# Kernel tuning notes

Hardware: AMD Instinct MI355X
Metric: run time of the kernel (lower is better)

Reference implementation:

```python
import jax, jax.numpy as jnp
import numpy as np

ALPHA = 0.2  # LeakyReLU negative slope
NEG_INF = -1.0e12


def setup_inputs() -> dict:
    key = jax.random.key(0)
    ks = jax.random.split(key, 8)
    N, F, D, H, M, Q = 4096, 512, 64, 4, 2, 128
    x = jax.random.normal(ks[0], (N, F), dtype=jnp.float32)
    adj = jax.random.randint(ks[1], (M, N, N), 0, 2, dtype=jnp.int32)
    W = jax.random.normal(ks[2], (H, F, D), dtype=jnp.float32) * 0.07
    a1 = jax.random.normal(ks[3], (H, D), dtype=jnp.float32) * 0.15
    a2 = jax.random.normal(ks[4], (H, D), dtype=jnp.float32) * 0.15
    Ws = jax.random.normal(ks[5], (H * D, Q), dtype=jnp.float32) * 0.1
    bs = jax.random.normal(ks[6], (1, Q), dtype=jnp.float32) * 0.1
    q_sem = jax.random.normal(ks[7], (Q, 1), dtype=jnp.float32) * 0.15
    return {"x": x, "adj": adj, "W": W, "a1": a1, "a2": a2,
            "Ws": Ws, "bs": bs, "q_sem": q_sem}


def reference(x, adj, W, a1, a2, Ws, bs, q_sem):
    N = x.shape[0]
    # Wh is identical across meta-paths (dropout disabled / eval mode)
    Wh = jnp.einsum('nf,hfd->hnd', x, W)            # [H,N,D]
    s1 = jnp.einsum('hnd,hd->hn', Wh, a1)           # Wh @ a[:D]
    s2 = jnp.einsum('hnd,hd->hn', Wh, a2)           # Wh @ a[D:]

    def metapath(adj_m):
        # e[h,i,j] = leaky_relu(s1[h,i] + s2[h,j]); mask by adjacency
        e = jax.nn.leaky_relu(s1[:, :, None] + s2[:, None, :], negative_slope=ALPHA)
        e = jnp.where(adj_m[None, :, :] > 0, e, NEG_INF)
        att = jax.nn.softmax(e, axis=2)             # softmax over neighbors (dim=1 in torch [N,N])
        h = jax.nn.elu(jnp.einsum('hnm,hmd->hnd', att, Wh))
        return jnp.transpose(h, (1, 0, 2)).reshape(N, -1)  # concat heads -> [N, H*D]

    Z = jax.vmap(metapath)(adj)                     # [M, N, H*D]
    z = jnp.transpose(Z, (1, 0, 2))                 # [N, M, H*D]

    # Semantic attention (faithful to original, incl. softmax over dim=1 of [M,1])
    Whs = jnp.tanh(jnp.einsum('nmf,fq->nmq', z, Ws) + bs)   # [N,M,Q]
    w = jnp.einsum('nmq,qo->nmo', Whs, q_sem).mean(0)        # [M,1]
    beta = jax.nn.softmax(w, axis=1)                          # [M,1]
    return (beta[None, :, :] * z).sum(axis=1)                 # [N, H*D]
```

## Files before the change

kernel.cpp:

```cpp
#include <hip/hip_runtime.h>
#include <hip/hip_fp16.h>
#include <stdint.h>

#define NN 4096
#define FF 512
#define DD 64
#define HH 4
#define MM 2
#define LOG2E 1.44269504088896340736f
#define ALPHA_LR 0.2f

typedef float f32x4 __attribute__((ext_vector_type(4)));
typedef _Float16 f16x8 __attribute__((ext_vector_type(8)));
typedef _Float16 f16x2 __attribute__((ext_vector_type(2)));
typedef unsigned short u16x2 __attribute__((ext_vector_type(2)));

extern "C" __device__ _Float16 __ocml_exp2_f16(_Float16);

union H4 { ushort4 u; _Float16 h[4]; };
union W8 { f16x8 v; uint32_t w[4]; f16x2 p[4]; };

__device__ inline float fast_exp2(float x) { return __builtin_amdgcn_exp2f(x); }
__device__ inline float fast_rcp(float x) { return __builtin_amdgcn_rcpf(x); }
__device__ inline f32x4 mfma16(f16x8 a, f16x8 b, f32x4 c) {
    return __builtin_amdgcn_mfma_f32_16x16x32_f16(a, b, c, 0, 0, 0);
}
__device__ inline uint32_t enc_f32(float f) {
    uint32_t u = __float_as_uint(f);
    return (u & 0x80000000u) ? ~u : (u | 0x80000000u);
}
__device__ inline float dec_f32(uint32_t k) {
    uint32_t u = (k & 0x80000000u) ? (k ^ 0x80000000u) : ~k;
    return __uint_as_float(u);
}
__device__ inline f16x2 msk01(uint32_t V, int k) {
    uint32_t w = (V >> (2 * k)) & 0x00010001u;
    u16x2 m = __builtin_bit_cast(u16x2, w) * (u16x2){0x3C00, 0x3C00};
    return __builtin_bit_cast(f16x2, m);
}
__device__ inline f16x2 pkmax(f16x2 a, f16x2 b) {
#if __has_builtin(__builtin_elementwise_max)
    return __builtin_elementwise_max(a, b);
#else
    return (f16x2){a[0] > b[0] ? a[0] : b[0], a[1] > b[1] ? a[1] : b[1]};
#endif
}

#define GLOAD_LDS(G, L)                                                     \
    __builtin_amdgcn_global_load_lds(                                       \
        (const __attribute__((address_space(1))) void*)(G),                 \
        (__attribute__((address_space(3))) void*)(L), 16, 0, 0)

__global__ __launch_bounds__(256) void k_prep(const int* __restrict__ adj,
                                              const float* __restrict__ W,
                                              _Float16* __restrict__ wt,
                                              unsigned long long* __restrict__ bitsT,
                                              uint32_t* __restrict__ m4a) {
    const int bid = blockIdx.x;
    if (bid < 2048) {
        const long long total = (long long)MM * NN * NN;
        const long long stride = 2048LL * 256;
        long long tid = (long long)bid * 256 + threadIdx.x;
        for (long long e = tid; e < total; e += stride) {
            unsigned long long msk = __ballot(adj[e] != 0);
            if ((threadIdx.x & 63) == 0) {
                long long q = e >> 6;
                int m  = (int)(q >> 18);
                int rem = (int)(q & 262143);
                int i  = rem >> 6;
                int jw = rem & 63;
                bitsT[((size_t)m * 64 + jw) * NN + i] = msk;
            }
        }
    } else {
        int t = (bid - 2048) * 256 + threadIdx.x;
        if (t < HH) m4a[t] = 0u;
        int c = t >> 9, f = t & 511;
        int h = c >> 6, d = c & 63;
        wt[t] = (_Float16)W[(h * FF + f) * DD + d];
    }
}

__global__ __launch_bounds__(512) void k_wh(const float* __restrict__ x,
                                            const _Float16* __restrict__ wt,
                                            const float* __restrict__ a1,
                                            const float* __restrict__ a2,
                                            _Float16* __restrict__ whT,
                                            float* __restrict__ s1L,
                                            _Float16* __restrict__ s2h,
                                            uint32_t* __restrict__ m4a) {
    __shared__ float sred[8][2][16];
    const int wave = threadIdx.x >> 6;
    const int h    = wave & 3;
    const int th   = wave >> 2;
    const int lane = threadIdx.x & 63;
    const int iL   = lane & 15;
    const int quad = lane >> 4;
    const int i0   = blockIdx.x * 16;

    f32x4 acc[2];
    acc[0] = (f32x4){0.f, 0.f, 0.f, 0.f};
    acc[1] = (f32x4){0.f, 0.f, 0.f, 0.f};

    const float* arow = x + (size_t)(i0 + iL) * FF + quad * 8;
    const _Float16* bbase = wt + (size_t)(h * 64 + th * 32 + iL) * FF + quad * 8;

    for (int kc = 0; kc < FF; kc += 32) {
        f32x4 xa = *(const f32x4*)(arow + kc);
        f32x4 xb = *(const f32x4*)(arow + kc + 4);
        f16x8 a;
        #pragma unroll
        for (int r = 0; r < 4; ++r) {
            a[r]     = (_Float16)xa[r];
            a[4 + r] = (_Float16)xb[r];
        }
        #pragma unroll
        for (int u = 0; u < 2; ++u) {
            f16x8 b = *(const f16x8*)(bbase + (size_t)(16 * u) * FF + kc);
            acc[u] = mfma16(a, b, acc[u]);
        }
    }
    #pragma unroll
    for (int u = 0; u < 2; ++u) {
        H4 o;
        #pragma unroll
        for (int r = 0; r < 4; ++r) o.h[r] = (_Float16)acc[u][r];
        *(ushort4*)(whT + (size_t)(h * 64 + th * 32 + 16 * u + iL) * NN + i0 + quad * 4) = o.u;
    }

    const float a1v0 = a1[h * 64 + th * 32 + iL];
    const float a1v1 = a1[h * 64 + th * 32 + 16 + iL];
    const float a2v0 = a2[h * 64 + th * 32 + iL];
    const float a2v1 = a2[h * 64 + th * 32 + 16 + iL];
    #pragma unroll
    for (int r = 0; r < 4; ++r) {
        float p1 = acc[0][r] * a1v0 + acc[1][r] * a1v1;
        float p2 = acc[0][r] * a2v0 + acc[1][r] * a2v1;
        #pragma unroll
        for (int off = 1; off < 16; off <<= 1) {
            p1 += __shfl_xor(p1, off);
            p2 += __shfl_xor(p2, off);
        }
        if (iL == 0) {
            sred[wave][0][quad * 4 + r] = p1;
            sred[wave][1][quad * 4 + r] = p2;
        }
    }
    __syncthreads();
    if (threadIdx.x < 64) {
        int h2  = threadIdx.x >> 4;
        int idx = threadIdx.x & 15;
        float s1 = sred[h2][0][idx] + sred[h2 + 4][0][idx];
        float s2 = sred[h2][1][idx] + sred[h2 + 4][1][idx];
        float s2l = s2 * LOG2E;
        s1L[h2 * NN + i0 + idx] = s1 * LOG2E;
        s2h[h2 * NN + i0 + idx] = (_Float16)s2l;
        float mx = s2l;
        #pragma unroll
        for (int off = 1; off < 16; off <<= 1) mx = fmaxf(mx, __shfl_xor(mx, off));
        if (idx == 0) atomicMax(m4a + h2, enc_f32(mx));
    }
}

__global__ __launch_bounds__(512, 1) void k_attn(const _Float16* __restrict__ whT,
                                                 const float* __restrict__ s1L,
                                                 const _Float16* __restrict__ s2h,
                                                 const uint32_t* __restrict__ m4a,
                                                 const unsigned long long* __restrict__ bitsT,
                                                 float* __restrict__ out) {
    union __align__(16) Smem {
        _Float16 stage[8][2][4096];
        struct {
            float xr[8][MM][4][16][16];
            float dr[8][MM][16];
        } epi;
    };
    __shared__ Smem sm;

    const int tid  = threadIdx.x;
    const int wave = tid >> 6;
    const int lane = tid & 63;
    const int iL   = lane & 15;
    const int quad = lane >> 4;
    const int h    = blockIdx.x & 3;
    const int i0   = (blockIdx.x >> 2) * 64;

    const float m4 = dec_f32(m4a[h]);
    f16x2 A2[4], B2[4];
    #pragma unroll
    for (int s = 0; s < 4; ++s) {
        float s1i = s1L[h * NN + i0 + 16 * s + iL];
        float vv  = s1i + m4;
        float cii = fmaxf(vv, ALPHA_LR * vv);
        _Float16 a = (_Float16)(s1i - cii);
        _Float16 b = (_Float16)(ALPHA_LR * s1i - cii);
        A2[s] = (f16x2){a, a};
        B2[s] = (f16x2){b, b};
    }
    const f16x2 al2 = (f16x2){(_Float16)ALPHA_LR, (_Float16)ALPHA_LR};

    f32x4 acc[4][MM][4];
    f32x4 accD[4][MM];
    #pragma unroll
    for (int s = 0; s < 4; ++s)
        #pragma unroll
        for (int m = 0; m < MM; ++m) {
            accD[s][m] = (f32x4){0.f, 0.f, 0.f, 0.f};
            #pragma unroll
            for (int t = 0; t < 4; ++t) acc[s][m][t] = (f32x4){0.f, 0.f, 0.f, 0.f};
        }

    f16x8 bones;
    #pragma unroll
    for (int e = 0; e < 8; ++e) bones[e] = (_Float16)1.0f;

    const _Float16* s2row = s2h + h * NN;
    const int qshift = quad * 8;
    const int jbase = wave * 512;

    const _Float16* stBase = whT
        + (size_t)(h * 64 + (lane >> 3)) * NN
        + (((lane & 7) ^ ((lane >> 3) & 7)) << 3);
    const int x3 = iL & 7;
    int rdOff[2];
    #pragma unroll
    for (int hf = 0; hf < 2; ++hf)
        rdOff[hf] = (iL << 7) + ((((hf << 2) + quad) ^ x3) << 4);

    _Float16* cur = &sm.stage[wave][0][0];
    _Float16* nxt = &sm.stage[wave][1][0];

    const unsigned long long* pB[MM][4];
    #pragma unroll
    for (int m = 0; m < MM; ++m)
        #pragma unroll
        for (int s = 0; s < 4; ++s)
            pB[m][s] = bitsT + (size_t)m * 64 * NN + i0 + 16 * s + iL;

    {
        const _Float16* src = stBase + jbase;
        #pragma unroll
        for (int k = 0; k < 8; ++k)
            GLOAD_LDS(src + (size_t)(k * 8) * NN, cur + k * 512);
    }
    asm volatile("s_waitcnt vmcnt(0)" ::: "memory");
    __builtin_amdgcn_sched_barrier(0);

    #pragma unroll 1
    for (int it = 0; it < 8; ++it) {
        const int jc = jbase + it * 64;
        const int jw = jc >> 6;
        unsigned long long bm[MM][4];
        #pragma unroll
        for (int m = 0; m < MM; ++m)
            #pragma unroll
            for (int s = 0; s < 4; ++s)
                bm[m][s] = pB[m][s][(size_t)jw * NN];
        W8 s2vh[2];
        s2vh[0].v = *(const f16x8*)(s2row + jc + qshift);
        s2vh[1].v = *(const f16x8*)(s2row + jc + 32 + qshift);

        __builtin_amdgcn_sched_barrier(0);
        if (it < 7) {
            const _Float16* src = stBase + (jc + 64);
            #pragma unroll
            for (int k = 0; k < 8; ++k)
                GLOAD_LDS(src + (size_t)(k * 8) * NN, nxt + k * 512);
        }
        __builtin_amdgcn_sched_barrier(0);

        #pragma unroll
        for (int half = 0; half < 2; ++half) {
            const int shft = 32 * half + qshift;
            f16x8 bfr[4];
            #pragma unroll
            for (int t = 0; t < 4; ++t)
                bfr[t] = *(const f16x8*)((const char*)cur + (t << 11) + rdOff[half]);

            #pragma unroll
            for (int s = 0; s < 4; ++s) {
                uint32_t rs0 = (uint32_t)(bm[0][s] >> shft) & 0xFFu;
                uint32_t rs1 = (uint32_t)(bm[1][s] >> shft) & 0xFFu;
                uint32_t V0 = rs0 | (rs0 << 15);
                uint32_t V1 = rs1 | (rs1 << 15);
                W8 a0, a1v;
                #pragma unroll
                for (int k = 0; k < 4; ++k) {
                    f16x2 z = s2vh[half].p[k] + A2[s];
                    f16x2 l = al2 * s2vh[half].p[k] + B2[s];
                    f16x2 mx = pkmax(z, l);
                    f16x2 p = (f16x2){__ocml_exp2_f16(mx[0]), __ocml_exp2_f16(mx[1])};
                    a0.p[k]  = p * msk01(V0, k);
                    a1v.p[k] = p * msk01(V1, k);
                }
                #pragma unroll
                for (int t = 0; t < 4; ++t) {
                    acc[s][0][t] = mfma16(a0.v, bfr[t], acc[s][0][t]);
                    acc[s][1][t] = mfma16(a1v.v, bfr[t], acc[s][1][t]);
                }
                accD[s][0] = mfma16(a0.v, bones, accD[s][0]);
                accD[s][1] = mfma16(a1v.v, bones, accD[s][1]);
            }
        }

        asm volatile("s_waitcnt vmcnt(0)" ::: "memory");
        __builtin_amdgcn_sched_barrier(0);
        _Float16* tmp = cur; cur = nxt; nxt = tmp;
    }

    #pragma unroll
    for (int s = 0; s < 4; ++s) {
        __syncthreads();
        #pragma unroll
        for (int m = 0; m < MM; ++m) {
            #pragma unroll
            for (int t = 0; t < 4; ++t)
                *(f32x4*)&sm.epi.xr[wave][m][t][iL][quad * 4] = acc[s][m][t];
            if (iL == 0) *(f32x4*)&sm.epi.dr[wave][m][quad * 4] = accD[s][m];
        }
        __syncthreads();
        if (wave < 4) {
            const int t = wave;
            f32x4 n0 = (f32x4){0.f, 0.f, 0.f, 0.f};
            f32x4 n1 = (f32x4){0.f, 0.f, 0.f, 0.f};
            f32x4 d0 = (f32x4){0.f, 0.f, 0.f, 0.f};
            f32x4 d1 = (f32x4){0.f, 0.f, 0.f, 0.f};
            #pragma unroll
            for (int sl = 0; sl < 8; ++sl) {
                n0 += *(const f32x4*)&sm.epi.xr[sl][0][t][iL][quad * 4];
                n1 += *(const f32x4*)&sm.epi.xr[sl][1][t][iL][quad * 4];
                d0 += *(const f32x4*)&sm.epi.dr[sl][0][quad * 4];
                d1 += *(const f32x4*)&sm.epi.dr[sl][1][quad * 4];
            }
            const int i0s = i0 + 16 * s;
            #pragma unroll
            for (int r = 0; r < 4; ++r) {
                float v0 = n0[r] * fast_rcp(d0[r]);
                float v1 = n1[r] * fast_rcp(d1[r]);
                float e0 = v0 > 0.f ? v0 : (fast_exp2(v0 * LOG2E) - 1.f);
                float e1 = v1 > 0.f ? v1 : (fast_exp2(v1 * LOG2E) - 1.f);
                out[(size_t)(i0s + quad * 4 + r) * (HH * DD) + h * 64 + 16 * t + iL] = e0 + e1;
            }
        }
    }
}

extern "C" void kernel_launch(void* const* d_in, const int* in_sizes, int n_in,
                              void* d_out, int out_size, void* d_ws, size_t ws_size,
                              hipStream_t stream) {
    const float* x   = (const float*)d_in[0];
    const int*   adj = (const int*)d_in[1];
    const float* W   = (const float*)d_in[2];
    const float* a1  = (const float*)d_in[3];
    const float* a2  = (const float*)d_in[4];
    float* out = (float*)d_out;

    char* ws = (char*)d_ws;
    _Float16* wt   = (_Float16*)(ws);
    _Float16* whT  = (_Float16*)(ws + 262144);
    float*    s1L  = (float*)(ws + 2359296);
    _Float16* s2h  = (_Float16*)(ws + 2424832);
    uint32_t* m4a  = (uint32_t*)(ws + 2457600);
    unsigned long long* bitsT = (unsigned long long*)(ws + 2490368);

    hipLaunchKernelGGL(k_prep, dim3(2560), dim3(256), 0, stream,
                       adj, W, wt, bitsT, m4a);
    hipLaunchKernelGGL(k_wh, dim3(256), dim3(512), 0, stream,
                       x, wt, a1, a2, whT, s1L, s2h, m4a);
    hipLaunchKernelGGL(k_attn, dim3(256), dim3(512), 0, stream,
                       whT, s1L, s2h, m4a, bitsT, out);
}
```

Measured before the change: 270.9 us.

## Factor attention exponent into precomputed per-row and per-column exp terms

Rewrites exp2(max(s1+s2 terms)) as max(U1[i]*e1[j], U2[i]*ea[j]), using the monotonicity of exp. The per-column factors exp2(s2-m) and exp2(alpha*(s2-m)) are computed once per wave into LDS, and the per-row factors once per thread. This removes two f16 transcendentals per score element from the inner loop, leaving packed multiplies and a max. The cost is extra LDS reads each half-iteration and a risk of fp16 underflow or precision loss in the products.

```diff
diff --git a/kernel.cpp b/kernel.cpp
--- a/kernel.cpp
+++ b/kernel.cpp
@@ -14,8 +14,6 @@
 typedef _Float16 f16x8 __attribute__((ext_vector_type(8)));
 typedef _Float16 f16x2 __attribute__((ext_vector_type(2)));
 typedef unsigned short u16x2 __attribute__((ext_vector_type(2)));
-
-extern "C" __device__ _Float16 __ocml_exp2_f16(_Float16);
 
 union H4 { ushort4 u; _Float16 h[4]; };
 union W8 { f16x8 v; uint32_t w[4]; f16x2 p[4]; };
@@ -168,12 +166,16 @@
                                                  const uint32_t* __restrict__ m4a,
                                                  const unsigned long long* __restrict__ bitsT,
                                                  float* __restrict__ out) {
-    union __align__(16) Smem {
-        _Float16 stage[8][2][4096];
-        struct {
-            float xr[8][MM][4][16][16];
-            float dr[8][MM][16];
-        } epi;
+    struct __align__(16) Smem {
+        union {
+            _Float16 stage[8][2][4096];
+            struct {
+                float xr[8][MM][4][16][16];
+                float dr[8][MM][16];
+            } epi;
+        };
+        _Float16 e1[8][512];
+        _Float16 ea[8][512];
     };
     __shared__ Smem sm;
 
@@ -185,19 +187,35 @@
     const int h    = blockIdx.x & 3;
     const int i0   = (blockIdx.x >> 2) * 64;
 
+    const int qshift = quad * 8;
+    const int jbase = wave * 512;
+
     const float m4 = dec_f32(m4a[h]);
-    f16x2 A2[4], B2[4];
+
+    {
+        f16x8 sv = *(const f16x8*)(s2h + h * NN + jbase + lane * 8);
+        f16x8 e1v8, eav8;
+        #pragma unroll
+        for (int e = 0; e < 8; ++e) {
+            float sf = (float)sv[e] - m4;
+            e1v8[e] = (_Float16)fast_exp2(sf);
+            eav8[e] = (_Float16)fast_exp2(ALPHA_LR * sf);
+        }
+        *(f16x8*)&sm.e1[wave][lane * 8] = e1v8;
+        *(f16x8*)&sm.ea[wave][lane * 8] = eav8;
+    }
+
+    f16x2 U1[4], U2[4];
     #pragma unroll
     for (int s = 0; s < 4; ++s) {
         float s1i = s1L[h * NN + i0 + 16 * s + iL];
         float vv  = s1i + m4;
         float cii = fmaxf(vv, ALPHA_LR * vv);
-        _Float16 a = (_Float16)(s1i - cii);
-        _Float16 b = (_Float16)(ALPHA_LR * s1i - cii);
-        A2[s] = (f16x2){a, a};
-        B2[s] = (f16x2){b, b};
-    }
-    const f16x2 al2 = (f16x2){(_Float16)ALPHA_LR, (_Float16)ALPHA_LR};
+        _Float16 a = (_Float16)fast_exp2(vv - cii);
+        _Float16 b = (_Float16)fast_exp2(ALPHA_LR * vv - cii);
+        U1[s] = (f16x2){a, a};
+        U2[s] = (f16x2){b, b};
+    }
 
     f32x4 acc[4][MM][4];
     f32x4 accD[4][MM];
@@ -213,10 +231,6 @@
     f16x8 bones;
     #pragma unroll
     for (int e = 0; e < 8; ++e) bones[e] = (_Float16)1.0f;
-
-    const _Float16* s2row = s2h + h * NN;
-    const int qshift = quad * 8;
-    const int jbase = wave * 512;
 
     const _Float16* stBase = whT
         + (size_t)(h * 64 + (lane >> 3)) * NN
@@ -256,9 +270,6 @@
             #pragma unroll
             for (int s = 0; s < 4; ++s)
                 bm[m][s] = pB[m][s][(size_t)jw * NN];
-        W8 s2vh[2];
-        s2vh[0].v = *(const f16x8*)(s2row + jc + qshift);
-        s2vh[1].v = *(const f16x8*)(s2row + jc + 32 + qshift);
 
         __builtin_amdgcn_sched_barrier(0);
         if (it < 7) {
@@ -272,6 +283,10 @@
         #pragma unroll
         for (int half = 0; half < 2; ++half) {
             const int shft = 32 * half + qshift;
+            const int eo = it * 64 + 32 * half + qshift;
+            W8 e1h_, eah_;
+            e1h_.v = *(const f16x8*)&sm.e1[wave][eo];
+            eah_.v = *(const f16x8*)&sm.ea[wave][eo];
             f16x8 bfr[4];
             #pragma unroll
             for (int t = 0; t < 4; ++t)
@@ -286,10 +301,9 @@
                 W8 a0, a1v;
                 #pragma unroll
                 for (int k = 0; k < 4; ++k) {
-                    f16x2 z = s2vh[half].p[k] + A2[s];
-                    f16x2 l = al2 * s2vh[half].p[k] + B2[s];
-                    f16x2 mx = pkmax(z, l);
-                    f16x2 p = (f16x2){__ocml_exp2_f16(mx[0]), __ocml_exp2_f16(mx[1])};
+                    f16x2 w1 = U1[s] * e1h_.p[k];
+                    f16x2 w2 = U2[s] * eah_.p[k];
+                    f16x2 p  = pkmax(w1, w2);
                     a0.p[k]  = p * msk01(V0, k);
                     a1v.p[k] = p * msk01(V1, k);
                 }
```

Result: no change. 267.4 us (-1.3%).
